# Performance work log

Hardware: AMD Instinct MI355X
Metric: run time of the kernel (lower is better)

The kernel has to match this reference:

```python
import math
import jax, jax.numpy as jnp
import numpy as np

LAYOUT = (64, 64, 1088, 5184)  # [text_end/startof0, startof0, startof1, endofall]
N_HEAD = 16
HIDDEN = 1024


def _offsets(kH, kW, causal):
    # row-major offsets of a centered kHxkW window; causal keeps the first
    # kH*kW//2+1 entries (all positions at or before the center in raster order)
    offs = [(a - kH // 2, b - kW // 2) for a in range(kH) for b in range(kW)]
    return offs[: kH * kW // 2 + 1] if causal else offs


def _shift(xp, rows0, cols0, di, dj, ph, pw):
    # xp: zero-padded [B,C,Hk+2ph,Wk+2pw]; gather key/value aligned to each query cell
    return xp[:, :, rows0 + di + ph, :][:, :, :, cols0 + dj + pw]


def f_similar(q, k, kH, kW, causal):
    # q: [B,C,Hq,Wq], k: [B,C,Hk,Wk] -> [B,Hq,Wq,K]; out-of-bound keys score 0
    Hq, Wq = q.shape[2], q.shape[3]
    Hk, Wk = k.shape[2], k.shape[3]
    ph, pw = kH // 2, kW // 2
    kp = jnp.pad(k, ((0, 0), (0, 0), (ph, ph), (pw, pw)))
    rows0 = jnp.arange(Hq) // (Hq // Hk)  # query cell -> key-grid center
    cols0 = jnp.arange(Wq) // (Wq // Wk)
    scores = [jnp.einsum('bchw,bchw->bhw', q, _shift(kp, rows0, cols0, di, dj, ph, pw))
              for (di, dj) in _offsets(kH, kW, causal)]
    return jnp.stack(scores, axis=-1)


def f_weighting(v, p, kH, kW, causal):
    # v: [B,C,Hk,Wk], p: [B,Hq,Wq,K] -> [B,C,Hq,Wq]; out-of-bound values are 0
    Hq, Wq = p.shape[1], p.shape[2]
    Hk, Wk = v.shape[2], v.shape[3]
    ph, pw = kH // 2, kW // 2
    vp = jnp.pad(v, ((0, 0), (0, 0), (ph, ph), (pw, pw)))
    rows0 = jnp.arange(Hq) // (Hq // Hk)
    cols0 = jnp.arange(Wq) // (Wq // Wk)
    out = jnp.zeros((v.shape[0], v.shape[1], Hq, Wq), v.dtype)
    for o, (di, dj) in enumerate(_offsets(kH, kW, causal)):
        out = out + p[..., o][:, None] * _shift(vp, rows0, cols0, di, dj, ph, pw)
    return out


def transpose_and_split(x, layout, n_head):
    b, s, h = x.shape
    c = h // n_head
    x = jnp.transpose(x, (0, 2, 1)).reshape(b * n_head, c, s)
    x_text = x[..., :layout[0]]
    s0 = int(math.isqrt(layout[2] - layout[1]))
    s1 = int(math.isqrt(layout[3] - layout[2]))
    x0 = x[..., layout[1]:layout[2]].reshape(b * n_head, c, s0, s0)
    x1 = x[..., layout[2]:layout[3]].reshape(b * n_head, c, s1, s1)
    return x, x_text, x0, x1


def sparse_attention_2d(q, k, v, n_head, layout, mask, ks, ks2):
    b, s, hn = q.shape
    c = hn // n_head
    bn = b * n_head
    t = layout[0]
    n0 = layout[2] - layout[1]
    n1 = layout[3] - layout[2]
    q = q * (1.0 / math.sqrt(c))
    q_all, q_text, q0, q1 = transpose_and_split(q, layout, n_head)
    k_all, k_text, k0, k1 = transpose_and_split(k, layout, n_head)
    v_all, v_text, v0, v1 = transpose_and_split(v, layout, n_head)

    # all queries -> text keys, masked
    m = mask[:, None]  # [b,1,s,t]
    sat = jnp.einsum('bci,bcj->bij', q_all, k_text).reshape(b, n_head, s, t)
    sat = (sat * m - 10000.0 * (1.0 - m)).reshape(bn, s, t)

    s00 = f_similar(q0, k0, ks, ks, True)    # [bn,32,32,ks*ks//2+1]
    s11 = f_similar(q1, k1, ks, ks, True)    # [bn,64,64,ks*ks//2+1]
    s10 = f_similar(q1, k0, ks2, ks2, False) # [bn,64,64,ks2*ks2]
    k00, k10, k11 = s00.shape[-1], s10.shape[-1], s11.shape[-1]

    probs_text = jax.nn.softmax(sat[:, :t], axis=-1)
    probs_0 = jax.nn.softmax(
        jnp.concatenate([sat[:, layout[1]:layout[2]], s00.reshape(bn, n0, k00)], axis=-1), axis=-1)
    probs_1 = jax.nn.softmax(
        jnp.concatenate([sat[:, layout[2]:layout[3]],
                         s10.reshape(bn, n1, k10),
                         s11.reshape(bn, n1, k11)], axis=-1), axis=-1)

    # all -> text context (layout[0]==layout[1] so the pad block is empty)
    probs_a2t = jnp.concatenate([probs_text, probs_0[:, :, :t], probs_1[:, :, :t]], axis=1)
    ctx_text = jnp.einsum('bhij,bhcj->bihc',
                          probs_a2t.reshape(b, n_head, s, t),
                          v_text.reshape(b, n_head, c, t)).reshape(b, s, hn)

    c00 = f_weighting(v0, probs_0[:, :, t:].reshape(s00.shape), ks, ks, True)
    c10 = f_weighting(v0, probs_1[:, :, t:t + k10].reshape(s10.shape), ks2, ks2, False)
    c11 = f_weighting(v1, probs_1[:, :, t + k10:].reshape(s11.shape), ks, ks, True)

    ctx_01 = jnp.concatenate([jnp.zeros((bn, c, layout[1]), q.dtype),
                              c00.reshape(bn, c, n0),
                              (c10 + c11).reshape(bn, c, n1)], axis=-1)
    ctx_01 = jnp.transpose(ctx_01.reshape(b, hn, s), (0, 2, 1))
    return ctx_text + ctx_01


def setup_inputs() -> dict:
    key = jax.random.key(0)
    ks = jax.random.split(key, 3)
    b, s, h, t = 4, LAYOUT[3], HIDDEN, LAYOUT[0]
    return {
        "hidden_states": jax.random.normal(ks[0], (b, s, h), jnp.float32),
        "mask": jnp.ones((b, s, t), jnp.float32),
        "w_qkv": jax.random.normal(ks[1], (h, 3 * h), jnp.float32) * 0.02,
        "b_qkv": jnp.zeros((3 * h,), jnp.float32),
        "w_out": jax.random.normal(ks[2], (h, h), jnp.float32) * 0.02,
        "b_out": jnp.zeros((h,), jnp.float32),
        "kernel_size": 9,
        "kernel_size2": 7,
    }


def reference(hidden_states, mask, w_qkv, b_qkv, w_out, b_out, kernel_size, kernel_size2):
    qkv = hidden_states @ w_qkv + b_qkv
    q, k, v = jnp.split(qkv, 3, axis=-1)
    ctx = sparse_attention_2d(q, k, v, N_HEAD, LAYOUT, mask, kernel_size, kernel_size2)
    return ctx @ w_out + b_out
```

## Files before the change

kernel.cpp:

```cpp
#include <hip/hip_runtime.h>
#include <hip/hip_bf16.h>

#define S_TOT 5184
#define S_PAD 5216
#define T_TXT 64
#define OFF0  64
#define OFF1  1088
#define NHEAD 16
#define CH    64
#define HID   1024
#define BATCH 4
#define BN_TOT (BATCH*NHEAD)
#define MTOT  (BATCH*S_TOT)
#define NIMG0 1024

typedef __attribute__((ext_vector_type(8))) short bf16x8;
typedef __attribute__((ext_vector_type(8))) _Float16 f16x8;
typedef __attribute__((ext_vector_type(4))) float f32x4;
typedef __attribute__((ext_vector_type(2))) _Float16 h2v;

__device__ __forceinline__ unsigned int f2bf(float x) {
  unsigned int u = __float_as_uint(x);
  unsigned int r = u + 0x7fffu + ((u >> 16) & 1u);
  return r >> 16;
}
__device__ __forceinline__ unsigned short f2h(float x) {
  _Float16 h = (_Float16)x;
  return __builtin_bit_cast(unsigned short, h);
}
__device__ __forceinline__ h2v h2(unsigned int u) { return __builtin_bit_cast(h2v, u); }
__device__ __forceinline__ float fd2(unsigned int a, unsigned int b, float c) {
  return __builtin_amdgcn_fdot2(h2(a), h2(b), c, false);
}
__device__ __forceinline__ unsigned int pklo(unsigned int a, unsigned int b) { return (a & 0xffffu) | (b << 16); }
__device__ __forceinline__ unsigned int pkhi(unsigned int a, unsigned int b) { return (a >> 16) | (b & 0xffff0000u); }
__device__ __forceinline__ f16x8 ld8h(const unsigned short* p) {
  return __builtin_bit_cast(f16x8, *(const uint4*)p);
}

__device__ __forceinline__ void gload_lds16(const short* g, short* l) {
  __builtin_amdgcn_global_load_lds(
      (const __attribute__((address_space(1))) unsigned int*)g,
      (__attribute__((address_space(3))) unsigned int*)l, 16, 0, 0);
}

__global__ __launch_bounds__(256) void cvt_bf16(const float* __restrict__ in,
                                                unsigned int* __restrict__ out, int n8) {
  const int i = blockIdx.x * 256 + threadIdx.x;
  if (i >= n8) return;
  const float4 a = ((const float4*)in)[2 * i];
  const float4 b = ((const float4*)in)[2 * i + 1];
  uint4 r;
  r.x = f2bf(a.x) | (f2bf(a.y) << 16);
  r.y = f2bf(a.z) | (f2bf(a.w) << 16);
  r.z = f2bf(b.x) | (f2bf(b.y) << 16);
  r.w = f2bf(b.z) | (f2bf(b.w) << 16);
  ((uint4*)out)[i] = r;
}

__global__ void cvt_T(const float* __restrict__ in, short* __restrict__ out,
                      const int R, const int Cn) {
  __shared__ float t[32][33];
  const int bx = blockIdx.x * 32, by = blockIdx.y * 32;
  const int tx = threadIdx.x, ty = threadIdx.y;
#pragma unroll
  for (int ph = 0; ph < 4; ++ph)
    t[ty + ph * 8][tx] = in[(size_t)(by + ty + ph * 8) * Cn + bx + tx];
  __syncthreads();
#pragma unroll
  for (int ph = 0; ph < 4; ++ph)
    out[(size_t)(bx + ty + ph * 8) * R + by + tx] = (short)f2bf(t[tx][ty + ph * 8]);
}

__global__ void cvt_Tv(const unsigned short* __restrict__ in, unsigned short* __restrict__ out) {
  __shared__ unsigned short t[32][33];
  const int bh = blockIdx.z;
  const int c0 = blockIdx.x * 32;
  const int s0 = blockIdx.y * 32;
  const int tx = threadIdx.x, ty = threadIdx.y;
  const unsigned short* src = in + (size_t)bh * S_TOT * CH;
  unsigned short* dst = out + (size_t)bh * CH * S_PAD;
#pragma unroll
  for (int ph = 0; ph < 4; ++ph)
    t[ty + ph * 8][tx] = src[(size_t)(s0 + ty + ph * 8) * CH + c0 + tx];
  __syncthreads();
#pragma unroll
  for (int ph = 0; ph < 4; ++ph)
    dst[(size_t)(c0 + ty + ph * 8) * S_PAD + s0 + tx] = t[tx][ty + ph * 8];
}

template<int EPI>
__global__ __launch_bounds__(256) void gemm_mfma(
    const short* __restrict__ A, const short* __restrict__ BT,
    const float* __restrict__ bias, float* __restrict__ C,
    unsigned short* __restrict__ qbuf, unsigned short* __restrict__ kbuf,
    unsigned short* __restrict__ vbuf,
    const int M, const int N, const int K)
{
  __shared__ short As[128 * 32];
  __shared__ short Bs[128 * 32];
  const int tid = threadIdx.x;
  const int w = tid >> 6, l = tid & 63;
  int lin = blockIdx.y * gridDim.x + blockIdx.x;
  const int nwg = gridDim.x * gridDim.y;
  lin = (lin & 7) * (nwg >> 3) + (lin >> 3);
  const int bm = (lin % gridDim.x) * 128;
  const int bn = (lin / gridDim.x) * 128;
  const int wr = w >> 1, wc = w & 1;
  const int lr = l & 15, lk = (l >> 4) * 8;

  const short* aSrc = A + (size_t)(bm + w * 32 + (l >> 2)) * K + (l & 3) * 8;
  const short* bSrc = BT + (size_t)(bn + w * 32 + (l >> 2)) * K + (l & 3) * 8;
  short* aDst = As + w * 32 * 32;
  short* bDst = Bs + w * 32 * 32;

  f32x4 acc[4][4];
#pragma unroll
  for (int m = 0; m < 4; ++m)
#pragma unroll
    for (int n = 0; n < 4; ++n) acc[m][n] = (f32x4){0.f, 0.f, 0.f, 0.f};

  for (int k0 = 0; k0 < K; k0 += 32) {
    gload_lds16(aSrc + k0,            aDst);
    gload_lds16(aSrc + k0 + 16 * K,   aDst + 16 * 32);
    gload_lds16(bSrc + k0,            bDst);
    gload_lds16(bSrc + k0 + 16 * K,   bDst + 16 * 32);
    __syncthreads();
    bf16x8 af[4], bfr[4];
#pragma unroll
    for (int m = 0; m < 4; ++m)
      af[m] = *(const bf16x8*)&As[(wr * 64 + m * 16 + lr) * 32 + lk];
#pragma unroll
    for (int n = 0; n < 4; ++n)
      bfr[n] = *(const bf16x8*)&Bs[(wc * 64 + n * 16 + lr) * 32 + lk];
#pragma unroll
    for (int m = 0; m < 4; ++m)
#pragma unroll
      for (int n = 0; n < 4; ++n)
        acc[m][n] = __builtin_amdgcn_mfma_f32_16x16x32_bf16(af[m], bfr[n], acc[m][n], 0, 0, 0);
    __syncthreads();
  }

#pragma unroll
  for (int m = 0; m < 4; ++m) {
    const int row0 = bm + wr * 64 + m * 16 + (l >> 4) * 4;
#pragma unroll
    for (int n = 0; n < 4; ++n) {
      const int col = bn + wc * 64 + n * 16 + lr;
      const float bv = bias[col];
      if constexpr (EPI == 0) {
#pragma unroll
        for (int i = 0; i < 4; ++i)
          C[(size_t)(row0 + i) * N + col] = acc[m][n][i] + bv;
      } else {
        const int type = col >> 10;
        const int head = (col & 1023) >> 6;
        const int chn  = col & 63;
        unsigned short* dst = (type == 0) ? qbuf : ((type == 1) ? kbuf : vbuf);
        const float sc = (type == 0) ? 0.125f : 1.f;
#pragma unroll
        for (int i = 0; i < 4; ++i) {
          const int row = row0 + i;
          const int b_ = row / S_TOT;
          const int s_ = row - b_ * S_TOT;
          dst[(((size_t)(b_ * NHEAD + head)) * S_TOT + s_) * CH + chn] =
              f2h((acc[m][n][i] + bv) * sc);
        }
      }
    }
  }
}

__global__ __launch_bounds__(256) __attribute__((amdgpu_waves_per_eu(2, 4)))
void attn_textpart(
    const unsigned short* __restrict__ qb, const unsigned short* __restrict__ kb,
    const unsigned short* __restrict__ vtf, const unsigned short* __restrict__ maskT,
    float* __restrict__ mT, float* __restrict__ lT, float* __restrict__ accT)
{
  __shared__ unsigned short ldsP[4][16][68];
  const int tid = threadIdx.x;
  const int w = tid >> 6, l = tid & 63;
  const int lr = l & 15, lg = l >> 4;
  const int bh = blockIdx.x >> 4;
  const int tile = (blockIdx.x & 15) * 4 + w;
  const int qs0 = OFF0 + tile * 16;
  const int b_ = bh >> 4;

  const unsigned short* qrow = qb + ((size_t)bh * S_TOT + qs0 + lr) * CH + lg * 8;
  const f16x8 aq0 = ld8h(qrow);
  const f16x8 aq1 = ld8h(qrow + 32);

  f32x4 s4[4];
  const unsigned short* kbase = kb + ((size_t)bh * S_TOT) * CH + lg * 8;
#pragma unroll
  for (int kt = 0; kt < 4; ++kt) {
    const unsigned short* krow = kbase + (kt * 16 + lr) * CH;
    f32x4 a = (f32x4){0.f, 0.f, 0.f, 0.f};
    a = __builtin_amdgcn_mfma_f32_16x16x32_f16(aq0, ld8h(krow), a, 0, 0, 0);
    a = __builtin_amdgcn_mfma_f32_16x16x32_f16(aq1, ld8h(krow + 32), a, 0, 0, 0);
    s4[kt] = a;
  }
#pragma unroll
  for (int kt = 0; kt < 4; ++kt) {
    const unsigned short* mrow = maskT + (size_t)(kt * 16 + lr) * MTOT + (size_t)b_ * S_TOT + qs0 + lg * 4;
#pragma unroll
    for (int i = 0; i < 4; ++i) {
      const float mv = __uint_as_float(((unsigned int)mrow[i]) << 16);
      s4[kt][i] = s4[kt][i] * mv - 10000.f * (1.f - mv);
    }
  }
  float mx[4], ls[4];
#pragma unroll
  for (int i = 0; i < 4; ++i) {
    float mxi = fmaxf(fmaxf(s4[0][i], s4[1][i]), fmaxf(s4[2][i], s4[3][i]));
    mxi = fmaxf(mxi, __shfl_xor(mxi, 1));
    mxi = fmaxf(mxi, __shfl_xor(mxi, 2));
    mxi = fmaxf(mxi, __shfl_xor(mxi, 4));
    mxi = fmaxf(mxi, __shfl_xor(mxi, 8));
    mx[i] = mxi;
    float li = 0.f;
#pragma unroll
    for (int kt = 0; kt < 4; ++kt) {
      const float p = __expf(s4[kt][i] - mxi);
      s4[kt][i] = p;
      li += p;
    }
    li += __shfl_xor(li, 1);
    li += __shfl_xor(li, 2);
    li += __shfl_xor(li, 4);
    li += __shfl_xor(li, 8);
    ls[i] = li;
  }
#pragma unroll
  for (int kt = 0; kt < 4; ++kt)
#pragma unroll
    for (int i = 0; i < 4; ++i)
      ldsP[w][lg * 4 + i][kt * 16 + lr] = f2h(s4[kt][i]);
  f16x8 ap[2];
#pragma unroll
  for (int c = 0; c < 2; ++c) {
    const unsigned short* pr = &ldsP[w][lr][lg * 8 + 32 * c];
    const uint2 x = *(const uint2*)pr;
    const uint2 y = *(const uint2*)(pr + 4);
    const uint4 u = make_uint4(x.x, x.y, y.x, y.y);
    ap[c] = __builtin_bit_cast(f16x8, u);
  }
  const size_t vrowbase = (size_t)bh * CH;
  const size_t qidx0 = (size_t)bh * NIMG0 + (qs0 - OFF0);
#pragma unroll
  for (int n = 0; n < 4; ++n) {
    const unsigned short* vrow = vtf + (vrowbase + n * 16 + lr) * S_PAD + lg * 8;
    f32x4 o = (f32x4){0.f, 0.f, 0.f, 0.f};
    o = __builtin_amdgcn_mfma_f32_16x16x32_f16(ap[0], ld8h(vrow), o, 0, 0, 0);
    o = __builtin_amdgcn_mfma_f32_16x16x32_f16(ap[1], ld8h(vrow + 32), o, 0, 0, 0);
#pragma unroll
    for (int i = 0; i < 4; ++i)
      accT[(qidx0 + lg * 4 + i) * 64 + n * 16 + lr] = o[i];
  }
  if (lr == 0) {
#pragma unroll
    for (int i = 0; i < 4; ++i) {
      mT[qidx0 + lg * 4 + i] = mx[i];
      lT[qidx0 + lg * 4 + i] = ls[i];
    }
  }
}

__global__ __launch_bounds__(256) __attribute__((amdgpu_waves_per_eu(2, 4)))
void attn_img1_mfma(
    const unsigned short* __restrict__ qb, const unsigned short* __restrict__ kb,
    const unsigned short* __restrict__ vtf, const unsigned short* __restrict__ maskT,
    short* __restrict__ ctx)
{
  __shared__ unsigned short ldsP[4][16][168];
  const int tid = threadIdx.x;
  const int w = tid >> 6, l = tid & 63;
  const int lr = l & 15, lg = l >> 4;
  const int bh = blockIdx.x >> 6;
  const int qi = blockIdx.x & 63;
  const int qj0 = w * 16;
  const int b_ = bh >> 4, head = bh & 15;
  const int s0 = OFF1 + qi * 64 + qj0;
  const size_t vrowbase = (size_t)bh * CH;
  unsigned short* myP = &ldsP[w][0][0];

  const unsigned short* qrow = qb + ((size_t)bh * S_TOT + s0 + lr) * CH + lg * 8;
  const f16x8 aq0 = ld8h(qrow);
  const f16x8 aq1 = ld8h(qrow + 32);

  float m[4], lsum[4];
  f32x4 acc[4];
#pragma unroll
  for (int i = 0; i < 4; ++i) { m[i] = -1e30f; lsum[i] = 0.f; }
#pragma unroll
  for (int n = 0; n < 4; ++n) acc[n] = (f32x4){0.f, 0.f, 0.f, 0.f};

  {
    f32x4 sC[4];
    const unsigned short* kb0 = kb + ((size_t)bh * S_TOT) * CH + lg * 8;
#pragma unroll
    for (int kt = 0; kt < 4; ++kt) {
      const unsigned short* krow = kb0 + (kt * 16 + lr) * CH;
      f32x4 a = (f32x4){0.f, 0.f, 0.f, 0.f};
      a = __builtin_amdgcn_mfma_f32_16x16x32_f16(aq0, ld8h(krow), a, 0, 0, 0);
      a = __builtin_amdgcn_mfma_f32_16x16x32_f16(aq1, ld8h(krow + 32), a, 0, 0, 0);
      sC[kt] = a;
    }
#pragma unroll
    for (int kt = 0; kt < 4; ++kt) {
      const unsigned short* mrow = maskT + (size_t)(kt * 16 + lr) * MTOT + (size_t)b_ * S_TOT + s0 + lg * 4;
#pragma unroll
      for (int i = 0; i < 4; ++i) {
        const float mv = __uint_as_float(((unsigned int)mrow[i]) << 16);
        sC[kt][i] = sC[kt][i] * mv - 10000.f * (1.f - mv);
      }
    }
    float rsc[4], la[4];
#pragma unroll
    for (int i = 0; i < 4; ++i) {
      float mx = fmaxf(fmaxf(sC[0][i], sC[1][i]), fmaxf(sC[2][i], sC[3][i]));
      mx = fmaxf(mx, __shfl_xor(mx, 1));
      mx = fmaxf(mx, __shfl_xor(mx, 2));
      mx = fmaxf(mx, __shfl_xor(mx, 4));
      mx = fmaxf(mx, __shfl_xor(mx, 8));
      const float mn = fmaxf(m[i], mx);
      rsc[i] = __expf(m[i] - mn);
      m[i] = mn;
      la[i] = 0.f;
    }
#pragma unroll
    for (int kt = 0; kt < 4; ++kt)
#pragma unroll
      for (int i = 0; i < 4; ++i) {
        const float p = __expf(sC[kt][i] - m[i]);
        la[i] += p;
        myP[(lg * 4 + i) * 168 + kt * 16 + lr] = f2h(p);
      }
#pragma unroll
    for (int i = 0; i < 4; ++i) {
      float li = la[i];
      li += __shfl_xor(li, 1);
      li += __shfl_xor(li, 2);
      li += __shfl_xor(li, 4);
      li += __shfl_xor(li, 8);
      lsum[i] = lsum[i] * rsc[i] + li;
#pragma unroll
      for (int n = 0; n < 4; ++n) acc[n][i] *= rsc[i];
    }
#pragma unroll
    for (int kt = 0; kt < 2; ++kt) {
      const f16x8 ap = __builtin_bit_cast(f16x8, *(const uint4*)&myP[lr * 168 + kt * 32 + lg * 8]);
      const int sbase = kt * 32 + lg * 8;
#pragma unroll
      for (int n = 0; n < 4; ++n) {
        const f16x8 bv = ld8h(vtf + (vrowbase + n * 16 + lr) * S_PAD + sbase);
        acc[n] = __builtin_amdgcn_mfma_f32_16x16x32_f16(ap, bv, acc[n], 0, 0, 0);
      }
    }
  }

  {
    const int ki0 = qi >> 1, cb = (qj0 >> 1) - 3;
    f32x4 sA[7];
#pragma unroll
    for (int rr = 0; rr < 7; ++rr) sA[rr] = (f32x4){-1e30f, -1e30f, -1e30f, -1e30f};
    const unsigned short* kbA = kb + ((size_t)bh * S_TOT + OFF0) * CH + lg * 8;
    const int kjc = min(max(cb + lr, 0), 31);
#pragma unroll
    for (int rr = 0; rr < 7; ++rr) {
      const int ki = ki0 + rr - 3;
      if ((unsigned)ki < 32u) {
        const unsigned short* krow = kbA + (ki * 32 + kjc) * CH;
        f32x4 a = (f32x4){0.f, 0.f, 0.f, 0.f};
        a = __builtin_amdgcn_mfma_f32_16x16x32_f16(aq0, ld8h(krow), a, 0, 0, 0);
        a = __builtin_amdgcn_mfma_f32_16x16x32_f16(aq1, ld8h(krow + 32), a, 0, 0, 0);
        sA[rr] = a;
      }
    }
    const int kjA = cb + lr;
    float pmax[4] = {-1e30f, -1e30f, -1e30f, -1e30f};
#pragma unroll
    for (int rr = 0; rr < 7; ++rr) {
      const int ki = ki0 + rr - 3;
      const bool rv = (unsigned)ki < 32u;
#pragma unroll
      for (int i = 0; i < 4; ++i) {
        const int kjq = (qj0 + lg * 4 + i) >> 1;
        const int dj = kjA - kjq;
        const bool ok = rv && dj >= -3 && dj <= 3 && kjA >= 0 && kjA < 32;
        sA[rr][i] = ok ? sA[rr][i] : -1e30f;
        pmax[i] = fmaxf(pmax[i], sA[rr][i]);
      }
    }
    float rsc[4], la[4];
#pragma unroll
    for (int i = 0; i < 4; ++i) {
      float mx = pmax[i];
      mx = fmaxf(mx, __shfl_xor(mx, 1));
      mx = fmaxf(mx, __shfl_xor(mx, 2));
      mx = fmaxf(mx, __shfl_xor(mx, 4));
      mx = fmaxf(mx, __shfl_xor(mx, 8));
      const float mn = fmaxf(m[i], mx);
      rsc[i] = __expf(m[i] - mn);
      m[i] = mn;
      la[i] = 0.f;
    }
#pragma unroll
    for (int rr = 0; rr < 7; ++rr)
#pragma unroll
      for (int i = 0; i < 4; ++i) {
        const float p = __expf(sA[rr][i] - m[i]);
        la[i] += p;
        myP[(lg * 4 + i) * 168 + rr * 16 + lr] = f2h(p);
      }
#pragma unroll
    for (int j2 = 0; j2 < 4; ++j2)
      myP[lr * 168 + 112 + lg * 4 + j2] = 0;
#pragma unroll
    for (int i = 0; i < 4; ++i) {
      float li = la[i];
      li += __shfl_xor(li, 1);
      li += __shfl_xor(li, 2);
      li += __shfl_xor(li, 4);
      li += __shfl_xor(li, 8);
      lsum[i] = lsum[i] * rsc[i] + li;
#pragma unroll
      for (int n = 0; n < 4; ++n) acc[n][i] *= rsc[i];
    }
#pragma unroll
    for (int kt = 0; kt < 4; ++kt) {
      const f16x8 ap = __builtin_bit_cast(f16x8, *(const uint4*)&myP[lr * 168 + kt * 32 + lg * 8]);
      const int rowidx = 2 * kt + (lg >> 1);
      const int kiv = min(max(ki0 + rowidx - 3, 0), 31);
      const int sbase = OFF0 + kiv * 32 + cb + (lg & 1) * 8;
#pragma unroll
      for (int n = 0; n < 4; ++n) {
        const f16x8 bv = ld8h(vtf + (vrowbase + n * 16 + lr) * S_PAD + sbase);
        acc[n] = __builtin_amdgcn_mfma_f32_16x16x32_f16(ap, bv, acc[n], 0, 0, 0);
      }
    }
  }

  {
    const int cbB = qj0 - 4;
    f32x4 sB[10];
#pragma unroll
    for (int rr = 0; rr < 10; ++rr) sB[rr] = (f32x4){-1e30f, -1e30f, -1e30f, -1e30f};
    const unsigned short* kbB = kb + ((size_t)bh * S_TOT + OFF1) * CH + lg * 8;
#pragma unroll
    for (int rr = 0; rr < 5; ++rr) {
      const int ki = qi + rr - 4;
      if (ki >= 0) {
#pragma unroll
        for (int t = 0; t < 2; ++t) {
          const int kjc = min(max(cbB + t * 16 + lr, 0), 63);
          const unsigned short* krow = kbB + (ki * 64 + kjc) * CH;
          f32x4 a = (f32x4){0.f, 0.f, 0.f, 0.f};
          a = __builtin_amdgcn_mfma_f32_16x16x32_f16(aq0, ld8h(krow), a, 0, 0, 0);
          a = __builtin_amdgcn_mfma_f32_16x16x32_f16(aq1, ld8h(krow + 32), a, 0, 0, 0);
          sB[rr * 2 + t] = a;
        }
      }
    }
    float pmax[4] = {-1e30f, -1e30f, -1e30f, -1e30f};
#pragma unroll
    for (int rr = 0; rr < 5; ++rr) {
      const int djmax = (rr == 4) ? 0 : 4;
#pragma unroll
      for (int t = 0; t < 2; ++t) {
        const int kj = cbB + t * 16 + lr;
#pragma unroll
        for (int i = 0; i < 4; ++i) {
          const int qj = qj0 + lg * 4 + i;
          const int dj = kj - qj;
          const bool ok = dj >= -4 && dj <= djmax && kj >= 0 && kj < 64;
          sB[rr * 2 + t][i] = ok ? sB[rr * 2 + t][i] : -1e30f;
          pmax[i] = fmaxf(pmax[i], sB[rr * 2 + t][i]);
        }
      }
    }
    float rsc[4], la[4];
#pragma unroll
    for (int i = 0; i < 4; ++i) {
      float mx = pmax[i];
      mx = fmaxf(mx, __shfl_xor(mx, 1));
      mx = fmaxf(mx, __shfl_xor(mx, 2));
      mx = fmaxf(mx, __shfl_xor(mx, 4));
      mx = fmaxf(mx, __shfl_xor(mx, 8));
      const float mn = fmaxf(m[i], mx);
      rsc[i] = __expf(m[i] - mn);
      m[i] = mn;
      la[i] = 0.f;
    }
#pragma unroll
    for (int rr = 0; rr < 5; ++rr)
#pragma unroll
      for (int t = 0; t < 2; ++t)
#pragma unroll
        for (int i = 0; i < 4; ++i) {
          const float p = __expf(sB[rr * 2 + t][i] - m[i]);
          la[i] += p;
          myP[(lg * 4 + i) * 168 + rr * 32 + t * 16 + lr] = f2h(p);
        }
#pragma unroll
    for (int i = 0; i < 4; ++i) {
      float li = la[i];
      li += __shfl_xor(li, 1);
      li += __shfl_xor(li, 2);
      li += __shfl_xor(li, 4);
      li += __shfl_xor(li, 8);
      lsum[i] = lsum[i] * rsc[i] + li;
#pragma unroll
      for (int n = 0; n < 4; ++n) acc[n][i] *= rsc[i];
    }
#pragma unroll
    for (int kt = 0; kt < 5; ++kt) {
      const f16x8 ap = __builtin_bit_cast(f16x8, *(const uint4*)&myP[lr * 168 + kt * 32 + lg * 8]);
      const int kiv = max(qi + kt - 4, 0);
      const int sbase = OFF1 + kiv * 64 + cbB + lg * 8;
#pragma unroll
      for (int n = 0; n < 4; ++n) {
        const f16x8 bv = ld8h(vtf + (vrowbase + n * 16 + lr) * S_PAD + sbase);
        acc[n] = __builtin_amdgcn_mfma_f32_16x16x32_f16(ap, bv, acc[n], 0, 0, 0);
      }
    }
  }

  const int ki0f = qi >> 1;
#pragma unroll
  for (int i = 0; i < 4; ++i) {
    const int qj = qj0 + lg * 4 + i;
    const int kjq = qj >> 1;
    const int nInvA = max(0, 3 - ki0f) + max(0, ki0f - 28);
    const int oobA  = max(0, 3 - kjq) + max(0, kjq - 28);
    const int nInvB = max(0, 4 - qi);
    const int oobB  = max(0, 4 - qj) + max(0, qj - 59);
    const int cnt = nInvA * 7 + (7 - nInvA) * oobA
                  + nInvB * 9 + (4 - nInvB) * oobB + max(0, 4 - qj);
    const float lf = lsum[i] + (float)cnt * __expf(-m[i]);
    const float inv = 1.f / lf;
    short* cp = ctx + ((size_t)(b_ * S_TOT) + s0 + lg * 4 + i) * HID + head * CH;
#pragma unroll
    for (int n = 0; n < 4; ++n)
      cp[n * 16 + lr] = (short)f2bf(acc[n][i] * inv);
  }
}

__device__ __forceinline__ float dot8h(const uint4 qd, const unsigned short* __restrict__ kp) {
  const uint4 a = *(const uint4*)kp;
  float s = 0.f;
  s = fd2(a.x, qd.x, s); s = fd2(a.y, qd.y, s);
  s = fd2(a.z, qd.z, s); s = fd2(a.w, qd.w, s);
  return s;
}
__device__ __forceinline__ void pv2d(float& a0, float& a1, unsigned int dA, unsigned int dB, h2v pp) {
  a0 = __builtin_amdgcn_fdot2(h2(pklo(dA, dB)), pp, a0, false);
  a1 = __builtin_amdgcn_fdot2(h2(pkhi(dA, dB)), pp, a1, false);
}
__device__ __forceinline__ void pv2q(float* __restrict__ acc, uint4 A, uint4 B, h2v pp) {
  pv2d(acc[0], acc[1], A.x, B.x, pp);
  pv2d(acc[2], acc[3], A.y, B.y, pp);
  pv2d(acc[4], acc[5], A.z, B.z, pp);
  pv2d(acc[6], acc[7], A.w, B.w, pp);
}

template<int W, bool MASKED>
__device__ __forceinline__ void row_upd(const uint4 qd,
                                        const unsigned short* __restrict__ krow,
                                        const unsigned short* __restrict__ vrow,
                                        const int kj0, const int limit,
                                        const unsigned short* __restrict__ maskT,
                                        const int rowIdx,
                                        float& m, float& l, float* __restrict__ acc, int& cnt) {
  float s[W];
#pragma unroll
  for (int j = 0; j < W; ++j) {
    const int kj = kj0 + j;
    const bool ok = (unsigned)kj < (unsigned)limit;
    float d = dot8h(qd, krow + (ok ? kj : 0) * CH);
    d += __shfl_xor(d, 1);
    d += __shfl_xor(d, 2);
    d += __shfl_xor(d, 4);
    if constexpr (MASKED) {
      const float mv = __uint_as_float(((unsigned int)maskT[(size_t)kj * MTOT + rowIdx]) << 16);
      s[j] = d * mv - 10000.f * (1.f - mv);
    } else {
      s[j] = ok ? d : -1e30f;
      cnt += ok ? 0 : 1;
    }
  }
  float smax = s[0];
#pragma unroll
  for (int j = 1; j < W; ++j) smax = fmaxf(smax, s[j]);
  const float mn = fmaxf(m, smax);
  const float r = __expf(m - mn);
  m = mn;
  l *= r;
#pragma unroll
  for (int i = 0; i < 8; ++i) acc[i] *= r;
  float p[W];
#pragma unroll
  for (int j = 0; j < W; ++j) { p[j] = __expf(s[j] - mn); l += p[j]; }
#pragma unroll
  for (int j = 0; j < W; j += 2) {
    const int kja = kj0 + j;
    const bool oka = (unsigned)kja < (unsigned)limit;
    const uint4 A = *(const uint4*)(vrow + (oka ? kja : 0) * CH);
    uint4 B; float pb;
    if (j + 1 < W) {
      const int kjb = kja + 1;
      const bool okb = (unsigned)kjb < (unsigned)limit;
      B = *(const uint4*)(vrow + (okb ? kjb : 0) * CH);
      pb = p[j + 1];
    } else {
      B = A; pb = 0.f;
    }
    const h2v pp = __builtin_bit_cast(h2v, __builtin_amdgcn_cvt_pkrtz(p[j], pb));
    pv2q(acc, A, B, pp);
  }
}

__device__ __forceinline__ void store_q8(short* ctx, size_t base,
                                         const float* acc, float inv) {
  unsigned int* cp = (unsigned int*)(ctx + base);
#pragma unroll
  for (int i = 0; i < 4; ++i)
    cp[i] = f2bf(acc[2 * i] * inv) | (f2bf(acc[2 * i + 1] * inv) << 16);
}

__global__ __launch_bounds__(256) __attribute__((amdgpu_waves_per_eu(4, 8)))
void attn_text(
    const unsigned short* __restrict__ qb, const unsigned short* __restrict__ kb,
    const unsigned short* __restrict__ vb, const unsigned short* __restrict__ maskT,
    short* __restrict__ ctx)
{
  const int t = blockIdx.x * 256 + threadIdx.x;
  const int oct = t & 7;
  const int qidx = t >> 3;
  const int bh = qidx >> 6;
  const int tq = qidx & 63;
  const int b_ = bh >> 4, head = bh & 15;

  const uint4 qd = *(const uint4*)(qb + ((size_t)bh * S_TOT + tq) * CH + oct * 8);

  float m = -1e30f, l = 0.f;
  float acc[8];
#pragma unroll
  for (int i = 0; i < 8; ++i) acc[i] = 0.f;
  int cnt = 0;

  const unsigned short* kt = kb + (size_t)bh * S_TOT * CH + oct * 8;
  const unsigned short* vt = vb + (size_t)bh * S_TOT * CH + oct * 8;
  const int rowIdx = b_ * S_TOT + tq;
  for (int t8 = 0; t8 < 8; ++t8)
    row_upd<8, true>(qd, kt, vt, t8 * 8, T_TXT, maskT, rowIdx, m, l, acc, cnt);
  store_q8(ctx, ((size_t)rowIdx) * HID + head * CH + oct * 8, acc, 1.f / l);
}

__global__ __launch_bounds__(256) __attribute__((amdgpu_waves_per_eu(4, 8)))
void attn_img0(
    const unsigned short* __restrict__ qb, const unsigned short* __restrict__ kb,
    const unsigned short* __restrict__ vb,
    const float* __restrict__ mT, const float* __restrict__ lT, const float* __restrict__ accT,
    short* __restrict__ ctx)
{
  const int t = blockIdx.x * 256 + threadIdx.x;
  const int oct = t & 7;
  const int qidx = t >> 3;
  const int bh = qidx >> 10;
  const int p = qidx & 1023;
  const int qi = p >> 5, qj = p & 31;
  const int s = OFF0 + p;
  const int b_ = bh >> 4, head = bh & 15;

  const uint4 qd = *(const uint4*)(qb + ((size_t)bh * S_TOT + s) * CH + oct * 8);

  const size_t qx = (size_t)bh * NIMG0 + p;
  float m = mT[qx];
  float l = lT[qx];
  float acc[8];
  {
    const float4* a4 = (const float4*)(accT + qx * 64 + oct * 8);
    const float4 A0 = a4[0], A1 = a4[1];
    acc[0] = A0.x; acc[1] = A0.y; acc[2] = A0.z; acc[3] = A0.w;
    acc[4] = A1.x; acc[5] = A1.y; acc[6] = A1.z; acc[7] = A1.w;
  }
  int cnt = 0;

  const unsigned short* kt = kb + (size_t)bh * S_TOT * CH + oct * 8;
  const unsigned short* vt = vb + (size_t)bh * S_TOT * CH + oct * 8;
  const unsigned short* k0 = kt + OFF0 * CH;
  const unsigned short* v0 = vt + OFF0 * CH;
#pragma unroll
  for (int di = -4; di <= -1; ++di) {
    const int ki = qi + di;
    if (ki >= 0)
      row_upd<9, false>(qd, k0 + ki * 32 * CH, v0 + ki * 32 * CH, qj - 4, 32,
                        nullptr, 0, m, l, acc, cnt);
    else cnt += 9;
  }
  row_upd<5, false>(qd, k0 + qi * 32 * CH, v0 + qi * 32 * CH, qj - 4, 32,
                    nullptr, 0, m, l, acc, cnt);

  l += (float)cnt * __expf(-m);
  store_q8(ctx, ((size_t)(b_ * S_TOT + s)) * HID + head * CH + oct * 8, acc, 1.f / l);
}

extern "C" void kernel_launch(void* const* d_in, const int* in_sizes, int n_in,
                              void* d_out, int out_size, void* d_ws, size_t ws_size,
                              hipStream_t stream) {
  const float* hidden = (const float*)d_in[0];
  const float* mask   = (const float*)d_in[1];
  const float* w_qkv  = (const float*)d_in[2];
  const float* b_qkv  = (const float*)d_in[3];
  const float* w_out  = (const float*)d_in[4];
  const float* b_out  = (const float*)d_in[5];
  float* out = (float*)d_out;

  const size_t NB = (size_t)BN_TOT * S_TOT * CH;
  unsigned short* qbuf = (unsigned short*)d_ws;
  unsigned short* kbuf = qbuf + NB;
  unsigned short* vbuf = kbuf + NB;
  short* hbf   = (short*)(vbuf + NB);
  short* wqkvT = hbf + NB;
  short* woutT = wqkvT + (size_t)3072 * 1024;
  short* maskT = woutT + (size_t)1024 * 1024;
  unsigned short* vtf = (unsigned short*)(maskT + (size_t)T_TXT * MTOT);
  float* mT   = (float*)(vtf + (size_t)BN_TOT * CH * S_PAD);
  float* lT   = mT + (size_t)BN_TOT * NIMG0;
  float* accT = lT + (size_t)BN_TOT * NIMG0;

  cvt_bf16<<<(int)((NB / 8 + 255) / 256), 256, 0, stream>>>(hidden, (unsigned int*)hbf, (int)(NB / 8));
  cvt_T<<<dim3(3072 / 32, 1024 / 32), dim3(32, 8), 0, stream>>>(w_qkv, wqkvT, 1024, 3072);
  cvt_T<<<dim3(1024 / 32, 1024 / 32), dim3(32, 8), 0, stream>>>(w_out, woutT, 1024, 1024);
  cvt_T<<<dim3(T_TXT / 32, MTOT / 32), dim3(32, 8), 0, stream>>>(mask, maskT, MTOT, T_TXT);

  gemm_mfma<1><<<dim3(MTOT / 128, 3072 / 128), 256, 0, stream>>>(
      hbf, wqkvT, b_qkv, nullptr, qbuf, kbuf, vbuf, MTOT, 3072, 1024);

  cvt_Tv<<<dim3(CH / 32, S_TOT / 32, BN_TOT), dim3(32, 8), 0, stream>>>(vbuf, vtf);

  short* ctx = hbf;
  attn_textpart<<<BN_TOT * 16, 256, 0, stream>>>(qbuf, kbuf, vtf, (unsigned short*)maskT,
                                                 mT, lT, accT);
  attn_text<<<(BN_TOT * T_TXT * 8) / 256, 256, 0, stream>>>(qbuf, kbuf, vbuf, (unsigned short*)maskT, ctx);
  attn_img0<<<(BN_TOT * 1024 * 8) / 256, 256, 0, stream>>>(qbuf, kbuf, vbuf, mT, lT, accT, ctx);
  attn_img1_mfma<<<BN_TOT * 64, 256, 0, stream>>>(qbuf, kbuf, vtf, (unsigned short*)maskT, ctx);

  gemm_mfma<0><<<dim3(MTOT / 128, 1024 / 128), 256, 0, stream>>>(
      ctx, woutT, b_out, out, nullptr, nullptr, nullptr, MTOT, 1024, 1024);
}
```

Before: 587.5 us.

## Fuse img0 text-part and local-window attention into one MFMA kernel

Replaces the two-stage img0 path (an MFMA text-part kernel writing m/l/acc partials to workspace plus a scalar fdot2 local-window kernel that reads them back) with a single MFMA kernel. Each wave computes text scores and banded 9x9 causal window scores with MFMA, masks them, runs one softmax and accumulates PV against the transposed V buffer. This removes one launch and the partial-state round trip through global memory, and moves the window dot products from scalar fdot2 onto matrix cores. The cost is wasted MFMA work on masked band entries, clamped redundant K loads, and a smaller 128-thread block.

```diff
diff --git a/kernel.cpp b/kernel.cpp
--- a/kernel.cpp
+++ b/kernel.cpp
@@ -12,7 +12,6 @@
 #define BATCH 4
 #define BN_TOT (BATCH*NHEAD)
 #define MTOT  (BATCH*S_TOT)
-#define NIMG0 1024
 
 typedef __attribute__((ext_vector_type(8))) short bf16x8;
 typedef __attribute__((ext_vector_type(8))) _Float16 f16x8;
@@ -172,101 +171,6 @@
 }
 
 __global__ __launch_bounds__(256) __attribute__((amdgpu_waves_per_eu(2, 4)))
-void attn_textpart(
-    const unsigned short* __restrict__ qb, const unsigned short* __restrict__ kb,
-    const unsigned short* __restrict__ vtf, const unsigned short* __restrict__ maskT,
-    float* __restrict__ mT, float* __restrict__ lT, float* __restrict__ accT)
-{
-  __shared__ unsigned short ldsP[4][16][68];
-  const int tid = threadIdx.x;
-  const int w = tid >> 6, l = tid & 63;
-  const int lr = l & 15, lg = l >> 4;
-  const int bh = blockIdx.x >> 4;
-  const int tile = (blockIdx.x & 15) * 4 + w;
-  const int qs0 = OFF0 + tile * 16;
-  const int b_ = bh >> 4;
-
-  const unsigned short* qrow = qb + ((size_t)bh * S_TOT + qs0 + lr) * CH + lg * 8;
-  const f16x8 aq0 = ld8h(qrow);
-  const f16x8 aq1 = ld8h(qrow + 32);
-
-  f32x4 s4[4];
-  const unsigned short* kbase = kb + ((size_t)bh * S_TOT) * CH + lg * 8;
-#pragma unroll
-  for (int kt = 0; kt < 4; ++kt) {
-    const unsigned short* krow = kbase + (kt * 16 + lr) * CH;
-    f32x4 a = (f32x4){0.f, 0.f, 0.f, 0.f};
-    a = __builtin_amdgcn_mfma_f32_16x16x32_f16(aq0, ld8h(krow), a, 0, 0, 0);
-    a = __builtin_amdgcn_mfma_f32_16x16x32_f16(aq1, ld8h(krow + 32), a, 0, 0, 0);
-    s4[kt] = a;
-  }
-#pragma unroll
-  for (int kt = 0; kt < 4; ++kt) {
-    const unsigned short* mrow = maskT + (size_t)(kt * 16 + lr) * MTOT + (size_t)b_ * S_TOT + qs0 + lg * 4;
-#pragma unroll
-    for (int i = 0; i < 4; ++i) {
-      const float mv = __uint_as_float(((unsigned int)mrow[i]) << 16);
-      s4[kt][i] = s4[kt][i] * mv - 10000.f * (1.f - mv);
-    }
-  }
-  float mx[4], ls[4];
-#pragma unroll
-  for (int i = 0; i < 4; ++i) {
-    float mxi = fmaxf(fmaxf(s4[0][i], s4[1][i]), fmaxf(s4[2][i], s4[3][i]));
-    mxi = fmaxf(mxi, __shfl_xor(mxi, 1));
-    mxi = fmaxf(mxi, __shfl_xor(mxi, 2));
-    mxi = fmaxf(mxi, __shfl_xor(mxi, 4));
-    mxi = fmaxf(mxi, __shfl_xor(mxi, 8));
-    mx[i] = mxi;
-    float li = 0.f;
-#pragma unroll
-    for (int kt = 0; kt < 4; ++kt) {
-      const float p = __expf(s4[kt][i] - mxi);
-      s4[kt][i] = p;
-      li += p;
-    }
-    li += __shfl_xor(li, 1);
-    li += __shfl_xor(li, 2);
-    li += __shfl_xor(li, 4);
-    li += __shfl_xor(li, 8);
-    ls[i] = li;
-  }
-#pragma unroll
-  for (int kt = 0; kt < 4; ++kt)
-#pragma unroll
-    for (int i = 0; i < 4; ++i)
-      ldsP[w][lg * 4 + i][kt * 16 + lr] = f2h(s4[kt][i]);
-  f16x8 ap[2];
-#pragma unroll
-  for (int c = 0; c < 2; ++c) {
-    const unsigned short* pr = &ldsP[w][lr][lg * 8 + 32 * c];
-    const uint2 x = *(const uint2*)pr;
-    const uint2 y = *(const uint2*)(pr + 4);
-    const uint4 u = make_uint4(x.x, x.y, y.x, y.y);
-    ap[c] = __builtin_bit_cast(f16x8, u);
-  }
-  const size_t vrowbase = (size_t)bh * CH;
-  const size_t qidx0 = (size_t)bh * NIMG0 + (qs0 - OFF0);
-#pragma unroll
-  for (int n = 0; n < 4; ++n) {
-    const unsigned short* vrow = vtf + (vrowbase + n * 16 + lr) * S_PAD + lg * 8;
-    f32x4 o = (f32x4){0.f, 0.f, 0.f, 0.f};
-    o = __builtin_amdgcn_mfma_f32_16x16x32_f16(ap[0], ld8h(vrow), o, 0, 0, 0);
-    o = __builtin_amdgcn_mfma_f32_16x16x32_f16(ap[1], ld8h(vrow + 32), o, 0, 0, 0);
-#pragma unroll
-    for (int i = 0; i < 4; ++i)
-      accT[(qidx0 + lg * 4 + i) * 64 + n * 16 + lr] = o[i];
-  }
-  if (lr == 0) {
-#pragma unroll
-    for (int i = 0; i < 4; ++i) {
-      mT[qidx0 + lg * 4 + i] = mx[i];
-      lT[qidx0 + lg * 4 + i] = ls[i];
-    }
-  }
-}
-
-__global__ __launch_bounds__(256) __attribute__((amdgpu_waves_per_eu(2, 4)))
 void attn_img1_mfma(
     const unsigned short* __restrict__ qb, const unsigned short* __restrict__ kb,
     const unsigned short* __restrict__ vtf, const unsigned short* __restrict__ maskT,
@@ -546,6 +450,168 @@
   }
 }
 
+__global__ __launch_bounds__(128) __attribute__((amdgpu_waves_per_eu(2, 4)))
+void attn_img0_mfma(
+    const unsigned short* __restrict__ qb, const unsigned short* __restrict__ kb,
+    const unsigned short* __restrict__ vtf, const unsigned short* __restrict__ maskT,
+    short* __restrict__ ctx)
+{
+  __shared__ unsigned short ldsP[2][16][168];
+  const int tid = threadIdx.x;
+  const int w = tid >> 6, l = tid & 63;
+  const int lr = l & 15, lg = l >> 4;
+  const int bh = blockIdx.x >> 5;
+  const int qi = blockIdx.x & 31;
+  const int qj0 = w * 16;
+  const int b_ = bh >> 4, head = bh & 15;
+  const int s0 = OFF0 + qi * 32 + qj0;
+  const size_t vrowbase = (size_t)bh * CH;
+  unsigned short* myP = &ldsP[w][0][0];
+
+  const unsigned short* qrow = qb + ((size_t)bh * S_TOT + s0 + lr) * CH + lg * 8;
+  const f16x8 aq0 = ld8h(qrow);
+  const f16x8 aq1 = ld8h(qrow + 32);
+
+  f32x4 sC[4];
+  {
+    const unsigned short* kb0 = kb + ((size_t)bh * S_TOT) * CH + lg * 8;
+#pragma unroll
+    for (int kt = 0; kt < 4; ++kt) {
+      const unsigned short* krow = kb0 + (kt * 16 + lr) * CH;
+      f32x4 a = (f32x4){0.f, 0.f, 0.f, 0.f};
+      a = __builtin_amdgcn_mfma_f32_16x16x32_f16(aq0, ld8h(krow), a, 0, 0, 0);
+      a = __builtin_amdgcn_mfma_f32_16x16x32_f16(aq1, ld8h(krow + 32), a, 0, 0, 0);
+      sC[kt] = a;
+    }
+  }
+  const int cbB = qj0 - 4;
+  f32x4 sB[10];
+  {
+#pragma unroll
+    for (int rr = 0; rr < 10; ++rr) sB[rr] = (f32x4){-1e30f, -1e30f, -1e30f, -1e30f};
+    const unsigned short* kbB = kb + ((size_t)bh * S_TOT + OFF0) * CH + lg * 8;
+#pragma unroll
+    for (int rr = 0; rr < 5; ++rr) {
+      const int ki = qi + rr - 4;
+      if (ki >= 0) {
+#pragma unroll
+        for (int t = 0; t < 2; ++t) {
+          const int kjc = min(max(cbB + t * 16 + lr, 0), 31);
+          const unsigned short* krow = kbB + (ki * 32 + kjc) * CH;
+          f32x4 a = (f32x4){0.f, 0.f, 0.f, 0.f};
+          a = __builtin_amdgcn_mfma_f32_16x16x32_f16(aq0, ld8h(krow), a, 0, 0, 0);
+          a = __builtin_amdgcn_mfma_f32_16x16x32_f16(aq1, ld8h(krow + 32), a, 0, 0, 0);
+          sB[rr * 2 + t] = a;
+        }
+      }
+    }
+  }
+
+#pragma unroll
+  for (int kt = 0; kt < 4; ++kt) {
+    const unsigned short* mrow = maskT + (size_t)(kt * 16 + lr) * MTOT + (size_t)b_ * S_TOT + s0 + lg * 4;
+#pragma unroll
+    for (int i = 0; i < 4; ++i) {
+      const float mv = __uint_as_float(((unsigned int)mrow[i]) << 16);
+      sC[kt][i] = sC[kt][i] * mv - 10000.f * (1.f - mv);
+    }
+  }
+#pragma unroll
+  for (int rr = 0; rr < 5; ++rr) {
+    const int djmax = (rr == 4) ? 0 : 4;
+#pragma unroll
+    for (int t = 0; t < 2; ++t) {
+      const int kj = cbB + t * 16 + lr;
+#pragma unroll
+      for (int i = 0; i < 4; ++i) {
+        const int qj = qj0 + lg * 4 + i;
+        const int dj = kj - qj;
+        const bool ok = dj >= -4 && dj <= djmax && kj >= 0 && kj < 32;
+        sB[rr * 2 + t][i] = ok ? sB[rr * 2 + t][i] : -1e30f;
+      }
+    }
+  }
+
+  float m[4], lsum[4];
+#pragma unroll
+  for (int i = 0; i < 4; ++i) {
+    float mx = fmaxf(fmaxf(sC[0][i], sC[1][i]), fmaxf(sC[2][i], sC[3][i]));
+#pragma unroll
+    for (int rr = 0; rr < 10; ++rr) mx = fmaxf(mx, sB[rr][i]);
+    mx = fmaxf(mx, __shfl_xor(mx, 1));
+    mx = fmaxf(mx, __shfl_xor(mx, 2));
+    mx = fmaxf(mx, __shfl_xor(mx, 4));
+    mx = fmaxf(mx, __shfl_xor(mx, 8));
+    m[i] = mx;
+    float li = 0.f;
+#pragma unroll
+    for (int kt = 0; kt < 4; ++kt) { const float p = __expf(sC[kt][i] - mx); sC[kt][i] = p; li += p; }
+#pragma unroll
+    for (int rr = 0; rr < 10; ++rr) { const float p = __expf(sB[rr][i] - mx); sB[rr][i] = p; li += p; }
+    li += __shfl_xor(li, 1);
+    li += __shfl_xor(li, 2);
+    li += __shfl_xor(li, 4);
+    li += __shfl_xor(li, 8);
+    lsum[i] = li;
+  }
+
+  f32x4 acc[4];
+#pragma unroll
+  for (int n = 0; n < 4; ++n) acc[n] = (f32x4){0.f, 0.f, 0.f, 0.f};
+
+  {
+#pragma unroll
+    for (int kt = 0; kt < 4; ++kt)
+#pragma unroll
+      for (int i = 0; i < 4; ++i)
+        myP[(lg * 4 + i) * 168 + kt * 16 + lr] = f2h(sC[kt][i]);
+#pragma unroll
+    for (int kt = 0; kt < 2; ++kt) {
+      const f16x8 ap = __builtin_bit_cast(f16x8, *(const uint4*)&myP[lr * 168 + kt * 32 + lg * 8]);
+      const int sbase = kt * 32 + lg * 8;
+#pragma unroll
+      for (int n = 0; n < 4; ++n) {
+        const f16x8 bv = ld8h(vtf + (vrowbase + n * 16 + lr) * S_PAD + sbase);
+        acc[n] = __builtin_amdgcn_mfma_f32_16x16x32_f16(ap, bv, acc[n], 0, 0, 0);
+      }
+    }
+  }
+  {
+#pragma unroll
+    for (int rr = 0; rr < 5; ++rr)
+#pragma unroll
+      for (int t = 0; t < 2; ++t)
+#pragma unroll
+        for (int i = 0; i < 4; ++i)
+          myP[(lg * 4 + i) * 168 + rr * 32 + t * 16 + lr] = f2h(sB[rr * 2 + t][i]);
+#pragma unroll
+    for (int kt = 0; kt < 5; ++kt) {
+      const f16x8 ap = __builtin_bit_cast(f16x8, *(const uint4*)&myP[lr * 168 + kt * 32 + lg * 8]);
+      const int kiv = max(qi + kt - 4, 0);
+      const int sbase = OFF0 + kiv * 32 + cbB + lg * 8;
+#pragma unroll
+      for (int n = 0; n < 4; ++n) {
+        const f16x8 bv = ld8h(vtf + (vrowbase + n * 16 + lr) * S_PAD + sbase);
+        acc[n] = __builtin_amdgcn_mfma_f32_16x16x32_f16(ap, bv, acc[n], 0, 0, 0);
+      }
+    }
+  }
+
+#pragma unroll
+  for (int i = 0; i < 4; ++i) {
+    const int qj = qj0 + lg * 4 + i;
+    const int nInvB = max(0, 4 - qi);
+    const int oobB  = max(0, 4 - qj) + max(0, qj - 27);
+    const int cnt = nInvB * 9 + (4 - nInvB) * oobB + max(0, 4 - qj);
+    const float lf = lsum[i] + (float)cnt * __expf(-m[i]);
+    const float inv = 1.f / lf;
+    short* cp = ctx + ((size_t)(b_ * S_TOT) + s0 + lg * 4 + i) * HID + head * CH;
+#pragma unroll
+    for (int n = 0; n < 4; ++n)
+      cp[n * 16 + lr] = (short)f2bf(acc[n][i] * inv);
+  }
+}
+
 __device__ __forceinline__ float dot8h(const uint4 qd, const unsigned short* __restrict__ kp) {
   const uint4 a = *(const uint4*)kp;
   float s = 0.f;
@@ -657,55 +723,6 @@
   store_q8(ctx, ((size_t)rowIdx) * HID + head * CH + oct * 8, acc, 1.f / l);
 }
 
-__global__ __launch_bounds__(256) __attribute__((amdgpu_waves_per_eu(4, 8)))
-void attn_img0(
-    const unsigned short* __restrict__ qb, const unsigned short* __restrict__ kb,
-    const unsigned short* __restrict__ vb,
-    const float* __restrict__ mT, const float* __restrict__ lT, const float* __restrict__ accT,
-    short* __restrict__ ctx)
-{
-  const int t = blockIdx.x * 256 + threadIdx.x;
-  const int oct = t & 7;
-  const int qidx = t >> 3;
-  const int bh = qidx >> 10;
-  const int p = qidx & 1023;
-  const int qi = p >> 5, qj = p & 31;
-  const int s = OFF0 + p;
-  const int b_ = bh >> 4, head = bh & 15;
-
-  const uint4 qd = *(const uint4*)(qb + ((size_t)bh * S_TOT + s) * CH + oct * 8);
-
-  const size_t qx = (size_t)bh * NIMG0 + p;
-  float m = mT[qx];
-  float l = lT[qx];
-  float acc[8];
-  {
-    const float4* a4 = (const float4*)(accT + qx * 64 + oct * 8);
-    const float4 A0 = a4[0], A1 = a4[1];
-    acc[0] = A0.x; acc[1] = A0.y; acc[2] = A0.z; acc[3] = A0.w;
-    acc[4] = A1.x; acc[5] = A1.y; acc[6] = A1.z; acc[7] = A1.w;
-  }
-  int cnt = 0;
-
-  const unsigned short* kt = kb + (size_t)bh * S_TOT * CH + oct * 8;
-  const unsigned short* vt = vb + (size_t)bh * S_TOT * CH + oct * 8;
-  const unsigned short* k0 = kt + OFF0 * CH;
-  const unsigned short* v0 = vt + OFF0 * CH;
-#pragma unroll
-  for (int di = -4; di <= -1; ++di) {
-    const int ki = qi + di;
-    if (ki >= 0)
-      row_upd<9, false>(qd, k0 + ki * 32 * CH, v0 + ki * 32 * CH, qj - 4, 32,
-                        nullptr, 0, m, l, acc, cnt);
-    else cnt += 9;
-  }
-  row_upd<5, false>(qd, k0 + qi * 32 * CH, v0 + qi * 32 * CH, qj - 4, 32,
-                    nullptr, 0, m, l, acc, cnt);
-
-  l += (float)cnt * __expf(-m);
-  store_q8(ctx, ((size_t)(b_ * S_TOT + s)) * HID + head * CH + oct * 8, acc, 1.f / l);
-}
-
 extern "C" void kernel_launch(void* const* d_in, const int* in_sizes, int n_in,
                               void* d_out, int out_size, void* d_ws, size_t ws_size,
                               hipStream_t stream) {
@@ -726,9 +743,6 @@
   short* woutT = wqkvT + (size_t)3072 * 1024;
   short* maskT = woutT + (size_t)1024 * 1024;
   unsigned short* vtf = (unsigned short*)(maskT + (size_t)T_TXT * MTOT);
-  float* mT   = (float*)(vtf + (size_t)BN_TOT * CH * S_PAD);
-  float* lT   = mT + (size_t)BN_TOT * NIMG0;
-  float* accT = lT + (size_t)BN_TOT * NIMG0;
 
   cvt_bf16<<<(int)((NB / 8 + 255) / 256), 256, 0, stream>>>(hidden, (unsigned int*)hbf, (int)(NB / 8));
   cvt_T<<<dim3(3072 / 32, 1024 / 32), dim3(32, 8), 0, stream>>>(w_qkv, wqkvT, 1024, 3072);
@@ -741,10 +755,8 @@
   cvt_Tv<<<dim3(CH / 32, S_TOT / 32, BN_TOT), dim3(32, 8), 0, stream>>>(vbuf, vtf);
 
   short* ctx = hbf;
-  attn_textpart<<<BN_TOT * 16, 256, 0, stream>>>(qbuf, kbuf, vtf, (unsigned short*)maskT,
-                                                 mT, lT, accT);
   attn_text<<<(BN_TOT * T_TXT * 8) / 256, 256, 0, stream>>>(qbuf, kbuf, vbuf, (unsigned short*)maskT, ctx);
-  attn_img0<<<(BN_TOT * 1024 * 8) / 256, 256, 0, stream>>>(qbuf, kbuf, vbuf, mT, lT, accT, ctx);
+  attn_img0_mfma<<<BN_TOT * 32, 128, 0, stream>>>(qbuf, kbuf, vtf, (unsigned short*)maskT, ctx);
   attn_img1_mfma<<<BN_TOT * 64, 256, 0, stream>>>(qbuf, kbuf, vtf, (unsigned short*)maskT, ctx);
 
   gemm_mfma<0><<<dim3(MTOT / 128, 1024 / 128), 256, 0, stream>>>(
```

After: 576.0 us. Within noise of the previous version (-2.0%).
